# Performance work log

Measured on AMD Instinct MI355X. Metric: run time of the kernel, lower is better.

The kernel has to match this reference:

```python
import jax, jax.numpy as jnp
import numpy as np

B, H, M, TK, NK, D = 4, 8, 1, 512, 511, 512
HD = D // H
NEG_INF = float('-inf')


def setup_inputs() -> dict:
    key = jax.random.key(0)
    ks = jax.random.split(key, 8)
    s = 0.02
    leaves = jax.random.normal(ks[0], (B, M, TK, D), jnp.float32)
    nodes = jax.random.normal(ks[1], (B, M, NK, D), jnp.float32)
    # per-head [left, right] leaf span of each tree node, left <= right
    node_indices = jnp.sort(jax.random.randint(ks[2], (B, H, M, NK, 2), 0, TK), axis=-1)
    key_pad = jnp.zeros((B, M, TK), jnp.bool_)
    node_pad = jnp.zeros((B, M, NK), jnp.bool_)
    Wq = jax.random.normal(ks[3], (D, D), jnp.float32) * s
    Wk = jax.random.normal(ks[4], (D, D), jnp.float32) * s
    Wv = jax.random.normal(ks[5], (D, D), jnp.float32) * s
    Wo = jax.random.normal(ks[6], (D, D), jnp.float32) * s
    bq = jnp.zeros((D,), jnp.float32)
    bk = jnp.zeros((D,), jnp.float32)
    bv = jnp.zeros((D,), jnp.float32)
    bo = jnp.zeros((D,), jnp.float32)
    return dict(leaves=leaves, nodes=nodes, Wq=Wq, Wk=Wk, Wv=Wv, Wo=Wo,
                bq=bq, bk=bk, bv=bv, bo=bo,
                node_indices=node_indices, key_pad=key_pad, node_pad=node_pad)


def _build_masks(node_indices, key_pad, node_pad):
    """Faithful jnp port of WeightMaskEff.build_mask_leaves_subtree."""
    L = M * (TK + NK)
    rg = jnp.arange(TK)
    # --- leaf queries: attend only non-pad leaves (node keys fully masked) ---
    leaf_mask = jnp.concatenate([key_pad, jnp.ones_like(node_pad)], axis=2)
    leaf_mask = leaf_mask.reshape(B, 1, 1, 1, L)                       # (B,1,1,1,L)
    # --- node queries over leaf keys: leaves inside the node's span ---
    idx_q = jnp.swapaxes(node_indices, 2, 3)                           # (B,H,NK,M,2)
    lo = idx_q[..., 0][..., None, None]                                # (B,H,NK,M,1,1)
    hi = idx_q[..., 1][..., None, None]
    leave_npad = (rg < lo) | (rg > hi)                                 # (B,H,NK,M,1,TK)
    leave_npad = leave_npad | jnp.swapaxes(node_pad, 1, 2)[:, None, :, :, None, None]
    leaf_keys_mask = leave_npad | key_pad[:, None, None, None, :, :]   # (B,H,NK,M,M,TK)
    # --- node queries over node keys: span overlap, lower-triangular ---
    in_span = (rg >= node_indices[..., 0:1]) & (rg <= node_indices[..., 1:2])  # (B,H,M,NK,TK)
    nl = in_span.astype(jnp.float32)
    overlap = jnp.tril(jnp.clip(jnp.einsum('bhmit,bhmjt->bhmij', nl, nl), 0.0, 1.0)) > 0
    node_npad = jnp.swapaxes(overlap[:, :, :, :, None, :], 2, 3)       # (B,H,NK,M,1,NK)
    node_keys_mask = (~node_npad) | node_pad[:, None, None, None, :, :]  # (B,H,NK,M,M,NK)
    node_mask = jnp.concatenate([leaf_keys_mask, node_keys_mask], axis=5).reshape(B, H, NK, M, L)
    return leaf_mask, node_mask


def _attention(leaves, nodes, Wq, Wk, Wv, Wo, bq, bk, bv, bo,
               node_indices, key_pad, node_pad):
    TKNK = TK + NK
    L = M * TKNK
    kv_src = jnp.concatenate([leaves, nodes], axis=2)        # (B,M,TKNK,D): key layout [m, tknk]
    q_src = jnp.swapaxes(kv_src, 1, 2).reshape(B, L, D)      # query layout [tknk, m]
    kv = kv_src.reshape(B, L, D)
    q = (q_src @ Wq.T + bq) * (HD ** -0.5)
    k = kv @ Wk.T + bk
    v = kv @ Wv.T + bv
    split = lambda x: jnp.swapaxes(x.reshape(B, L, H, HD), 1, 2)  # (B,H,L,HD)
    qh, kh, vh = split(q), split(k), split(v)
    w = jnp.einsum('bhqd,bhkd->bhqk', qh, kh).reshape(B, H, TKNK, M, L)
    leaf_mask, node_mask = _build_masks(node_indices, key_pad, node_pad)
    w = jnp.concatenate([
        jnp.where(leaf_mask, NEG_INF, w[:, :, :TK]),
        jnp.where(node_mask, NEG_INF, w[:, :, TK:]),
    ], axis=2).reshape(B, H, L, L)
    p = jax.nn.softmax(w, axis=-1)
    out = jnp.einsum('bhqk,bhkd->bhqd', p, vh)
    out = jnp.swapaxes(out, 1, 2).reshape(B, L, D)
    return out @ Wo.T + bo


def reference(leaves, nodes, Wq, Wk, Wv, Wo, bq, bk, bv, bo,
              node_indices, key_pad, node_pad):
    return _attention(leaves, nodes, Wq, Wk, Wv, Wo, bq, bk, bv, bo,
                      node_indices, key_pad, node_pad)
```

## Files before the change

kernel.cpp:

```cpp
#include <hip/hip_runtime.h>
#include <math.h>

#define Bn 4
#define Hn 8
#define TKn 512
#define NKn 511
#define Dn 512
#define HDn 64
#define Ln 1023
#define ROWSn (Bn * Ln)
#define NEG_SENT (-1.0e30f)

typedef __attribute__((ext_vector_type(8))) short short8;
typedef __attribute__((ext_vector_type(4))) short short4v;
typedef __attribute__((ext_vector_type(4))) float f32x4;
typedef unsigned short ushort_t;

__device__ __forceinline__ ushort_t f2bf(float f) {
    union { float f; unsigned int u; } v; v.f = f;
    unsigned int r = v.u + 0x7FFF + ((v.u >> 16) & 1);
    return (ushort_t)(r >> 16);
}
__device__ __forceinline__ unsigned int pk2(float a, float b) {
    return (unsigned int)f2bf(a) | ((unsigned int)f2bf(b) << 16);
}

#define LEAF_U ((Bn * TKn * Dn) / 8)
#define NODE_U ((Bn * NKn * Dn) / 8)
#define W_U    ((Dn * Dn) / 8)
__global__ __launch_bounds__(256) void convert_kernel(
    const float* __restrict__ leaves, const float* __restrict__ nodes,
    const float* __restrict__ Wq, const float* __restrict__ Wk,
    const float* __restrict__ Wv, const float* __restrict__ Wo,
    ushort_t* __restrict__ Xb, ushort_t* __restrict__ Wb)
{
    int u = blockIdx.x * 256 + threadIdx.x;
    const float* src;
    ushort_t* dst;
    if (u < LEAF_U) {
        int e = u * 8;
        int b = e / (TKn * Dn);
        int rem = e - b * (TKn * Dn);
        src = leaves + e;
        dst = Xb + (size_t)b * Ln * Dn + rem;
    } else if (u < LEAF_U + NODE_U) {
        int e = (u - LEAF_U) * 8;
        int b = e / (NKn * Dn);
        int rem = e - b * (NKn * Dn);
        src = nodes + e;
        dst = Xb + ((size_t)b * Ln + TKn) * Dn + rem;
    } else {
        int e = u - LEAF_U - NODE_U;
        int w = e / W_U;
        int rem = (e - w * W_U) * 8;
        src = (w == 0 ? Wq : w == 1 ? Wk : w == 2 ? Wv : Wo) + rem;
        dst = Wb + (size_t)w * Dn * Dn + rem;
    }
    float4 f0 = *(const float4*)src;
    float4 f1 = *(const float4*)(src + 4);
    int4 o;
    o.x = (int)pk2(f0.x, f0.y);
    o.y = (int)pk2(f0.z, f0.w);
    o.z = (int)pk2(f1.x, f1.y);
    o.w = (int)pk2(f1.z, f1.w);
    *(int4*)dst = o;
}

__global__ __launch_bounds__(256) void qkv_mfma_kernel(
    const ushort_t* __restrict__ Xb, const ushort_t* __restrict__ Wb,
    const float* __restrict__ bq, const float* __restrict__ bk, const float* __restrict__ bv,
    ushort_t* __restrict__ Qo, ushort_t* __restrict__ Ko, ushort_t* __restrict__ Vt)
{
    const int col0g = blockIdx.y * 64;
    const int which = col0g >> 9;
    const int colm  = col0g & 511;
    const ushort_t* __restrict__ W = Wb + (size_t)which * Dn * Dn;
    const float* __restrict__ bias = (which == 0) ? bq : (which == 1) ? bk : bv;
    const float scale = (which == 0) ? 0.125f : 1.0f;

    __shared__ ushort_t As[128][72];
    __shared__ ushort_t Bs[64][72];

    const int tid = threadIdx.x;
    const int lane = tid & 63, wave = tid >> 6;
    const int ln = lane & 15, quad = lane >> 4;
    const int wm = wave & 1, wn = wave >> 1;
    const int row0 = blockIdx.x * 128;

    f32x4 acc[2][4];
    #pragma unroll
    for (int i = 0; i < 2; ++i)
        #pragma unroll
        for (int j = 0; j < 4; ++j) acc[i][j] = (f32x4){0.f, 0.f, 0.f, 0.f};

    for (int k0 = 0; k0 < Dn; k0 += 64) {
        #pragma unroll
        for (int s = 0; s < 4; ++s) {
            int e = tid + s * 256;
            int r = e >> 3, c = (e & 7) * 8;
            int row = row0 + r;
            *(int4*)&As[r][c] = (row < ROWSn)
                ? *(const int4*)&Xb[(size_t)row * Dn + k0 + c] : (int4){0, 0, 0, 0};
        }
        #pragma unroll
        for (int s = 0; s < 2; ++s) {
            int e = tid + s * 256;
            int r = e >> 3, c = (e & 7) * 8;
            *(int4*)&Bs[r][c] = *(const int4*)&W[(size_t)(colm + r) * Dn + k0 + c];
        }
        __syncthreads();

        #pragma unroll
        for (int kc = 0; kc < 2; ++kc) {
            short8 af[2], bf[4];
            #pragma unroll
            for (int ni = 0; ni < 2; ++ni)
                af[ni] = *(const short8*)&Bs[wn * 32 + ni * 16 + ln][kc * 32 + quad * 8];
            #pragma unroll
            for (int mi = 0; mi < 4; ++mi)
                bf[mi] = *(const short8*)&As[wm * 64 + mi * 16 + ln][kc * 32 + quad * 8];
            #pragma unroll
            for (int ni = 0; ni < 2; ++ni)
                #pragma unroll
                for (int mi = 0; mi < 4; ++mi)
                    acc[ni][mi] = __builtin_amdgcn_mfma_f32_16x16x32_bf16(af[ni], bf[mi], acc[ni][mi], 0, 0, 0);
        }
        __syncthreads();
    }

    if (which == 2) {
        const int h = colm >> 6;
        #pragma unroll
        for (int ni = 0; ni < 2; ++ni) {
            const int d0 = wn * 32 + ni * 16 + quad * 4;
            const float4 b4 = *(const float4*)&bias[colm + d0];
            #pragma unroll
            for (int mi = 0; mi < 4; ++mi) {
                int row = row0 + wm * 64 + mi * 16 + ln;
                if (row >= ROWSn) continue;
                int bb = row / Ln;
                int l  = row - bb * Ln;
                size_t vbase = ((size_t)((bb * Hn + h) * HDn + d0)) * 1024 + l;
                Vt[vbase]        = f2bf(acc[ni][mi][0] + b4.x);
                Vt[vbase + 1024] = f2bf(acc[ni][mi][1] + b4.y);
                Vt[vbase + 2048] = f2bf(acc[ni][mi][2] + b4.z);
                Vt[vbase + 3072] = f2bf(acc[ni][mi][3] + b4.w);
            }
        }
    } else {
        ushort_t* __restrict__ Y = (which == 0) ? Qo : Ko;
        #pragma unroll
        for (int ni = 0; ni < 2; ++ni) {
            const int colb = colm + wn * 32 + ni * 16 + quad * 4;
            const float4 b4 = *(const float4*)&bias[colb];
            #pragma unroll
            for (int mi = 0; mi < 4; ++mi) {
                int row = row0 + wm * 64 + mi * 16 + ln;
                if (row >= ROWSn) continue;
                uint2 o;
                o.x = pk2(scale * (acc[ni][mi][0] + b4.x), scale * (acc[ni][mi][1] + b4.y));
                o.y = pk2(scale * (acc[ni][mi][2] + b4.z), scale * (acc[ni][mi][3] + b4.w));
                *(uint2*)&Y[(size_t)row * Dn + colb] = o;
            }
        }
    }
}

__global__ __launch_bounds__(256) void outproj_mfma_kernel(
    const ushort_t* __restrict__ AOb, const ushort_t* __restrict__ Wb,
    const float* __restrict__ bo, float* __restrict__ out)
{
    const ushort_t* __restrict__ W = Wb + (size_t)3 * Dn * Dn;
    __shared__ ushort_t As[64][136];
    __shared__ ushort_t Bs[64][136];

    const int tid = threadIdx.x;
    const int lane = tid & 63, wave = tid >> 6;
    const int ln = lane & 15, quad = lane >> 4;
    const int wm = wave & 1, wn = wave >> 1;
    const int row0 = blockIdx.x * 64;
    const int col0 = blockIdx.y * 64;

    f32x4 acc[2][2];
    #pragma unroll
    for (int i = 0; i < 2; ++i)
        #pragma unroll
        for (int j = 0; j < 2; ++j) acc[i][j] = (f32x4){0.f, 0.f, 0.f, 0.f};

    for (int k0 = 0; k0 < Dn; k0 += 128) {
        #pragma unroll
        for (int s = 0; s < 4; ++s) {
            int e = tid + s * 256;
            int r = e >> 4, c = (e & 15) * 8;
            int row = row0 + r;
            *(int4*)&As[r][c] = (row < ROWSn)
                ? *(const int4*)&AOb[(size_t)row * Dn + k0 + c] : (int4){0, 0, 0, 0};
            *(int4*)&Bs[r][c] = *(const int4*)&W[(size_t)(col0 + r) * Dn + k0 + c];
        }
        __syncthreads();

        #pragma unroll
        for (int kc = 0; kc < 4; ++kc) {
            short8 af[2], bf[2];
            #pragma unroll
            for (int ni = 0; ni < 2; ++ni)
                af[ni] = *(const short8*)&Bs[wn * 32 + ni * 16 + ln][kc * 32 + quad * 8];
            #pragma unroll
            for (int mi = 0; mi < 2; ++mi)
                bf[mi] = *(const short8*)&As[wm * 32 + mi * 16 + ln][kc * 32 + quad * 8];
            #pragma unroll
            for (int ni = 0; ni < 2; ++ni)
                #pragma unroll
                for (int mi = 0; mi < 2; ++mi)
                    acc[ni][mi] = __builtin_amdgcn_mfma_f32_16x16x32_bf16(af[ni], bf[mi], acc[ni][mi], 0, 0, 0);
        }
        __syncthreads();
    }

    #pragma unroll
    for (int ni = 0; ni < 2; ++ni) {
        const int colb = col0 + wn * 32 + ni * 16 + quad * 4;
        const float4 b4 = *(const float4*)&bo[colb];
        #pragma unroll
        for (int mi = 0; mi < 2; ++mi) {
            int row = row0 + wm * 32 + mi * 16 + ln;
            if (row >= ROWSn) continue;
            float4 o;
            o.x = acc[ni][mi][0] + b4.x;
            o.y = acc[ni][mi][1] + b4.y;
            o.z = acc[ni][mi][2] + b4.z;
            o.w = acc[ni][mi][3] + b4.w;
            *(float4*)&out[(size_t)row * Dn + colb] = o;
        }
    }
}

__global__ __launch_bounds__(256) void attn_mfma_kernel(
    const ushort_t* __restrict__ Qb, const ushort_t* __restrict__ Kb,
    const ushort_t* __restrict__ Vt, const int* __restrict__ nodeidx,
    ushort_t* __restrict__ AOb)
{
    const int qtile = 15 - (int)blockIdx.x;
    const int h = blockIdx.y, b = blockIdx.z;
    const int tid = threadIdx.x;
    const int lane = tid & 63, wave = tid >> 6;
    const int ln = lane & 15, quad = lane >> 4;
    const bool leafq = qtile < 8;
    const int ktend = leafq ? 8 : qtile + 1;

    __shared__ ushort_t Ks[64][72];
    __shared__ ushort_t Vts[64][72];
    __shared__ int2 nsp[512];

    const int nbase = (b * Hn + h) * NKn * 2;
    if (!leafq) {
        int i = tid;
        nsp[i] = (i < NKn) ? *(const int2*)&nodeidx[nbase + 2 * i] : (int2){0, -1};
        i = tid + 256;
        nsp[i] = (i < NKn) ? *(const int2*)&nodeidx[nbase + 2 * i] : (int2){0, -1};
    }

    const int q0 = qtile * 64;
    const int rq = q0 + wave * 16 + ln;
    const ushort_t* qp = Qb + ((size_t)(b * Ln + rq)) * Dn + h * HDn + quad * 8;
    const short8 qf0 = *(const short8*)qp;
    const short8 qf1 = *(const short8*)(qp + 32);

    const bool qvalid = rq < Ln;
    const int iq = rq - TKn;
    int qlo = 0, qhi = -1;
    if (!leafq && qvalid) {
        int2 t = *(const int2*)&nodeidx[nbase + 2 * iq];
        qlo = t.x; qhi = t.y;
    }

    float m_run = NEG_SENT, l_run = 0.f;
    f32x4 O[4];
    #pragma unroll
    for (int nd = 0; nd < 4; ++nd) O[nd] = (f32x4){0.f, 0.f, 0.f, 0.f};

    const size_t kbgl = (size_t)(b * Ln) * Dn + h * HDn;
    const ushort_t* Vp = Vt + (size_t)((b * Hn + h) * HDn) * 1024;

    for (int kt = 0; kt < ktend; ++kt) {
        const int k0 = kt * 64;
        if (kt) __syncthreads();
        #pragma unroll
        for (int s = 0; s < 2; ++s) {
            int e = tid + s * 256;
            int r = e >> 3, c = (e & 7) * 8;
            int key = k0 + r;
            *(int4*)&Ks[r][c] = (key < Ln)
                ? *(const int4*)&Kb[kbgl + (size_t)key * Dn + c] : (int4){0, 0, 0, 0};
            *(int4*)&Vts[r][c] = *(const int4*)&Vp[(size_t)r * 1024 + k0 + c];
        }
        __syncthreads();

        f32x4 st[4];
        #pragma unroll
        for (int n = 0; n < 4; ++n) {
            short8 kf0 = *(const short8*)&Ks[n * 16 + ln][quad * 8];
            short8 kf1 = *(const short8*)&Ks[n * 16 + ln][32 + quad * 8];
            f32x4 s = __builtin_amdgcn_mfma_f32_16x16x32_bf16(kf0, qf0,
                        (f32x4){0.f, 0.f, 0.f, 0.f}, 0, 0, 0);
            st[n] = __builtin_amdgcn_mfma_f32_16x16x32_bf16(kf1, qf1, s, 0, 0, 0);
        }

        if (!leafq) {
            if (k0 < TKn) {
                #pragma unroll
                for (int n = 0; n < 4; ++n) {
                    int keyb = k0 + n * 16 + quad * 4;
                    #pragma unroll
                    for (int r = 0; r < 4; ++r) {
                        int key = keyb + r;
                        bool a = (key >= qlo) && (key <= qhi);
                        st[n][r] = a ? st[n][r] : NEG_SENT;
                    }
                }
            } else {
                #pragma unroll
                for (int n = 0; n < 4; ++n) {
                    int idx = k0 + n * 16 + quad * 4 - TKn;
                    int4 sa = *(const int4*)&nsp[idx];
                    int4 sb = *(const int4*)&nsp[idx + 2];
                    bool a0 = (idx + 0 <= iq) && (sa.x <= qhi) && (qlo <= sa.y);
                    bool a1 = (idx + 1 <= iq) && (sa.z <= qhi) && (qlo <= sa.w);
                    bool a2 = (idx + 2 <= iq) && (sb.x <= qhi) && (qlo <= sb.y);
                    bool a3 = (idx + 3 <= iq) && (sb.z <= qhi) && (qlo <= sb.w);
                    st[n][0] = a0 ? st[n][0] : NEG_SENT;
                    st[n][1] = a1 ? st[n][1] : NEG_SENT;
                    st[n][2] = a2 ? st[n][2] : NEG_SENT;
                    st[n][3] = a3 ? st[n][3] : NEG_SENT;
                }
            }
        }

        float mx = NEG_SENT;
        #pragma unroll
        for (int n = 0; n < 4; ++n)
            #pragma unroll
            for (int r = 0; r < 4; ++r) mx = fmaxf(mx, st[n][r]);
        mx = fmaxf(mx, __shfl_xor(mx, 16));
        mx = fmaxf(mx, __shfl_xor(mx, 32));

        float mn = fmaxf(m_run, mx);
        float alpha = __expf(m_run - mn);
        m_run = mn;

        float lsum = 0.f;
        short4v ap[4];
        #pragma unroll
        for (int n = 0; n < 4; ++n) {
            float p[4];
            #pragma unroll
            for (int r = 0; r < 4; ++r) {
                float sv = st[n][r];
                p[r] = (sv == NEG_SENT) ? 0.f : __expf(sv - mn);
                lsum += p[r];
            }
            ap[n] = (short4v){(short)f2bf(p[0]), (short)f2bf(p[1]),
                              (short)f2bf(p[2]), (short)f2bf(p[3])};
        }
        lsum += __shfl_xor(lsum, 16);
        lsum += __shfl_xor(lsum, 32);
        l_run = l_run * alpha + lsum;

        float alr[4];
        #pragma unroll
        for (int r = 0; r < 4; ++r) alr[r] = __shfl(alpha, quad * 4 + r);
        #pragma unroll
        for (int nd = 0; nd < 4; ++nd)
            #pragma unroll
            for (int r = 0; r < 4; ++r) O[nd][r] *= alr[r];

        #pragma unroll
        for (int c = 0; c < 4; ++c) {
            #pragma unroll
            for (int nd = 0; nd < 4; ++nd) {
                short4v bv = *(const short4v*)&Vts[nd * 16 + ln][c * 16 + quad * 4];
                O[nd] = __builtin_amdgcn_mfma_f32_16x16x16bf16_1k(ap[c], bv, O[nd], 0, 0, 0);
            }
        }
    }

    float lr[4];
    #pragma unroll
    for (int r = 0; r < 4; ++r) lr[r] = __shfl(l_run, quad * 4 + r);
    #pragma unroll
    for (int r = 0; r < 4; ++r) {
        int rqr = q0 + wave * 16 + quad * 4 + r;
        if (rqr >= Ln) continue;
        float inv = 1.f / lr[r];
        size_t base = (size_t)(b * Ln + rqr) * Dn + h * HDn;
        #pragma unroll
        for (int nd = 0; nd < 4; ++nd)
            AOb[base + nd * 16 + ln] = f2bf(O[nd][r] * inv);
    }
}

extern "C" void kernel_launch(void* const* d_in, const int* in_sizes, int n_in,
                              void* d_out, int out_size, void* d_ws, size_t ws_size,
                              hipStream_t stream)
{
    const float* leaves = (const float*)d_in[0];
    const float* nodes  = (const float*)d_in[1];
    const float* Wq = (const float*)d_in[2];
    const float* Wk = (const float*)d_in[3];
    const float* Wv = (const float*)d_in[4];
    const float* Wo = (const float*)d_in[5];
    const float* bq = (const float*)d_in[6];
    const float* bk = (const float*)d_in[7];
    const float* bv = (const float*)d_in[8];
    const float* bo = (const float*)d_in[9];
    const int* nodeidx = (const int*)d_in[10];

    ushort_t* ws = (ushort_t*)d_ws;
    const size_t N = (size_t)ROWSn * Dn;
    ushort_t* Xb  = ws;
    ushort_t* Wb  = Xb + N;
    ushort_t* Qb  = Wb + (size_t)4 * Dn * Dn;
    ushort_t* Kb  = Qb + N;
    ushort_t* Vt  = Kb + N;
    ushort_t* AOb = Vt + (size_t)Bn * Hn * HDn * 1024;

    convert_kernel<<<1535, 256, 0, stream>>>(leaves, nodes, Wq, Wk, Wv, Wo, Xb, Wb);

    dim3 pgrid(32, 24);
    qkv_mfma_kernel<<<pgrid, 256, 0, stream>>>(Xb, Wb, bq, bk, bv, Qb, Kb, Vt);

    dim3 agrid(16, Hn, Bn);
    attn_mfma_kernel<<<agrid, 256, 0, stream>>>(Qb, Kb, Vt, nodeidx, AOb);

    dim3 ogrid(64, 8);
    outproj_mfma_kernel<<<ogrid, 256, 0, stream>>>(AOb, Wb, bo, (float*)d_out);
}
```

Baseline: 156.2 us.

## Split attention key tiles across waves with 16-row query blocks and XCD-aware mapping

The attention kernel now gives each block 16 query rows instead of 64. Its four waves split the key tiles among themselves, flash-decoding style, and their partial max, sum and O values are merged through shared memory at the end. K and V fragments are read straight from global memory, so the shared-memory staging and the per-tile barriers are gone. The 1D grid of 2048 blocks is mapped so that each XCD handles a few (batch, head) pairs, which should help L2 reuse and balance work across causal tiles. The cost is more total global/L2 traffic, since K and V are reloaded per block with no LDS reuse, plus a shared-memory reduction epilogue.

```diff
diff --git a/kernel.cpp b/kernel.cpp
--- a/kernel.cpp
+++ b/kernel.cpp
@@ -240,17 +240,21 @@
     const ushort_t* __restrict__ Vt, const int* __restrict__ nodeidx,
     ushort_t* __restrict__ AOb)
 {
-    const int qtile = 15 - (int)blockIdx.x;
-    const int h = blockIdx.y, b = blockIdx.z;
+    const int lb = blockIdx.x;
+    const int xcd = lb & 7, u = lb >> 3;
+    const int bh = xcd * 4 + (u >> 6);
+    const int qg = 63 - (u & 63);
+    const int b = bh >> 3, h = bh & 7;
     const int tid = threadIdx.x;
     const int lane = tid & 63, wave = tid >> 6;
     const int ln = lane & 15, quad = lane >> 4;
-    const bool leafq = qtile < 8;
-    const int ktend = leafq ? 8 : qtile + 1;
-
-    __shared__ ushort_t Ks[64][72];
-    __shared__ ushort_t Vts[64][72];
+    const int q0 = qg * 16;
+    const bool leafq = q0 < TKn;
+    const int ktend = leafq ? 8 : ((q0 + 16 + 63) >> 6);
+
     __shared__ int2 nsp[512];
+    __shared__ float Osh[4][64][17];
+    __shared__ float msh[4][16], lsh[4][16];
 
     const int nbase = (b * Hn + h) * NKn * 2;
     if (!leafq) {
@@ -258,11 +262,12 @@
         nsp[i] = (i < NKn) ? *(const int2*)&nodeidx[nbase + 2 * i] : (int2){0, -1};
         i = tid + 256;
         nsp[i] = (i < NKn) ? *(const int2*)&nodeidx[nbase + 2 * i] : (int2){0, -1};
-    }
-
-    const int q0 = qtile * 64;
-    const int rq = q0 + wave * 16 + ln;
-    const ushort_t* qp = Qb + ((size_t)(b * Ln + rq)) * Dn + h * HDn + quad * 8;
+        __syncthreads();
+    }
+
+    const int rq = q0 + ln;
+    const int rqc = (rq < Ln) ? rq : (Ln - 1);
+    const ushort_t* qp = Qb + ((size_t)(b * Ln + rqc)) * Dn + h * HDn + quad * 8;
     const short8 qf0 = *(const short8*)qp;
     const short8 qf1 = *(const short8*)(qp + 32);
 
@@ -279,28 +284,20 @@
     #pragma unroll
     for (int nd = 0; nd < 4; ++nd) O[nd] = (f32x4){0.f, 0.f, 0.f, 0.f};
 
-    const size_t kbgl = (size_t)(b * Ln) * Dn + h * HDn;
+    const ushort_t* Kp = Kb + (size_t)(b * Ln) * Dn + h * HDn;
     const ushort_t* Vp = Vt + (size_t)((b * Hn + h) * HDn) * 1024;
 
-    for (int kt = 0; kt < ktend; ++kt) {
+    for (int kt = wave; kt < ktend; kt += 4) {
         const int k0 = kt * 64;
-        if (kt) __syncthreads();
-        #pragma unroll
-        for (int s = 0; s < 2; ++s) {
-            int e = tid + s * 256;
-            int r = e >> 3, c = (e & 7) * 8;
-            int key = k0 + r;
-            *(int4*)&Ks[r][c] = (key < Ln)
-                ? *(const int4*)&Kb[kbgl + (size_t)key * Dn + c] : (int4){0, 0, 0, 0};
-            *(int4*)&Vts[r][c] = *(const int4*)&Vp[(size_t)r * 1024 + k0 + c];
-        }
-        __syncthreads();
 
         f32x4 st[4];
         #pragma unroll
         for (int n = 0; n < 4; ++n) {
-            short8 kf0 = *(const short8*)&Ks[n * 16 + ln][quad * 8];
-            short8 kf1 = *(const short8*)&Ks[n * 16 + ln][32 + quad * 8];
+            int krow = k0 + n * 16 + ln;
+            if (krow > Ln - 1) krow = Ln - 1;
+            const ushort_t* kp = Kp + (size_t)krow * Dn + quad * 8;
+            short8 kf0 = *(const short8*)kp;
+            short8 kf1 = *(const short8*)(kp + 32);
             f32x4 s = __builtin_amdgcn_mfma_f32_16x16x32_bf16(kf0, qf0,
                         (f32x4){0.f, 0.f, 0.f, 0.f}, 0, 0, 0);
             st[n] = __builtin_amdgcn_mfma_f32_16x16x32_bf16(kf1, qf1, s, 0, 0, 0);
@@ -378,24 +375,34 @@
         for (int c = 0; c < 4; ++c) {
             #pragma unroll
             for (int nd = 0; nd < 4; ++nd) {
-                short4v bv = *(const short4v*)&Vts[nd * 16 + ln][c * 16 + quad * 4];
+                short4v bv = *(const short4v*)&Vp[(size_t)(nd * 16 + ln) * 1024
+                                                  + k0 + c * 16 + quad * 4];
                 O[nd] = __builtin_amdgcn_mfma_f32_16x16x16bf16_1k(ap[c], bv, O[nd], 0, 0, 0);
             }
         }
     }
 
-    float lr[4];
-    #pragma unroll
-    for (int r = 0; r < 4; ++r) lr[r] = __shfl(l_run, quad * 4 + r);
-    #pragma unroll
-    for (int r = 0; r < 4; ++r) {
-        int rqr = q0 + wave * 16 + quad * 4 + r;
-        if (rqr >= Ln) continue;
-        float inv = 1.f / lr[r];
-        size_t base = (size_t)(b * Ln + rqr) * Dn + h * HDn;
-        #pragma unroll
-        for (int nd = 0; nd < 4; ++nd)
-            AOb[base + nd * 16 + ln] = f2bf(O[nd][r] * inv);
+    if (lane < 16) { msh[wave][lane] = m_run; lsh[wave][lane] = l_run; }
+    #pragma unroll
+    for (int nd = 0; nd < 4; ++nd)
+        #pragma unroll
+        for (int r = 0; r < 4; ++r)
+            Osh[wave][nd * 16 + ln][quad * 4 + r] = O[nd][r];
+    __syncthreads();
+
+    const int d = tid & 63;
+    #pragma unroll
+    for (int qq = tid >> 6; qq < 16; qq += 4) {
+        int rqq = q0 + qq;
+        if (rqq >= Ln) continue;
+        float m0 = msh[0][qq], m1 = msh[1][qq], m2 = msh[2][qq], m3 = msh[3][qq];
+        float M = fmaxf(fmaxf(m0, m1), fmaxf(m2, m3));
+        float e0 = __expf(m0 - M), e1 = __expf(m1 - M);
+        float e2 = __expf(m2 - M), e3 = __expf(m3 - M);
+        float L = lsh[0][qq] * e0 + lsh[1][qq] * e1 + lsh[2][qq] * e2 + lsh[3][qq] * e3;
+        float acc = Osh[0][d][qq] * e0 + Osh[1][d][qq] * e1
+                  + Osh[2][d][qq] * e2 + Osh[3][d][qq] * e3;
+        AOb[(size_t)(b * Ln + rqq) * Dn + h * HDn + d] = f2bf(acc / L);
     }
 }
 
@@ -429,8 +436,7 @@
     dim3 pgrid(32, 24);
     qkv_mfma_kernel<<<pgrid, 256, 0, stream>>>(Xb, Wb, bq, bk, bv, Qb, Kb, Vt);
 
-    dim3 agrid(16, Hn, Bn);
-    attn_mfma_kernel<<<agrid, 256, 0, stream>>>(Qb, Kb, Vt, nodeidx, AOb);
+    attn_mfma_kernel<<<2048, 256, 0, stream>>>(Qb, Kb, Vt, nodeidx, AOb);
 
     dim3 ogrid(64, 8);
     outproj_mfma_kernel<<<ogrid, 256, 0, stream>>>(AOb, Wb, bo, (float*)d_out);
```

Result: slower. 185.7 us (+18.9%).

## Double-buffer K/V tiles with register prefetch and split attention into smaller blocks

Applied to the files above, without the earlier changes.

The attention kernel now uses 128-thread blocks over 32-query tiles, launched as a flat grid of 1024 blocks with the heaviest tiles scheduled first. K/V tiles are prefetched into registers one step ahead and stored into double-buffered shared memory, so each iteration needs one barrier instead of two and global loads overlap with MFMA work. The shared-memory row padding changes to 70, and the convert kernel now zeroes the padding column of the transposed V buffer. The aim is more blocks for load balancing across CUs and hidden load latency, at the cost of higher register pressure and K/V reloaded once per 32 queries instead of per 64.

```diff
diff --git a/kernel.cpp b/kernel.cpp
--- a/kernel.cpp
+++ b/kernel.cpp
@@ -32,9 +32,11 @@
     const float* __restrict__ leaves, const float* __restrict__ nodes,
     const float* __restrict__ Wq, const float* __restrict__ Wk,
     const float* __restrict__ Wv, const float* __restrict__ Wo,
-    ushort_t* __restrict__ Xb, ushort_t* __restrict__ Wb)
+    ushort_t* __restrict__ Xb, ushort_t* __restrict__ Wb,
+    ushort_t* __restrict__ Vtz)
 {
     int u = blockIdx.x * 256 + threadIdx.x;
+    if (u < Bn * Hn * HDn) Vtz[(size_t)u * 1024 + 1023] = 0;
     const float* src;
     ushort_t* dst;
     if (u < LEAF_U) {
@@ -235,34 +237,39 @@
     }
 }
 
-__global__ __launch_bounds__(256) void attn_mfma_kernel(
+__global__ __launch_bounds__(128) void attn_mfma_kernel(
     const ushort_t* __restrict__ Qb, const ushort_t* __restrict__ Kb,
     const ushort_t* __restrict__ Vt, const int* __restrict__ nodeidx,
     ushort_t* __restrict__ AOb)
 {
-    const int qtile = 15 - (int)blockIdx.x;
-    const int h = blockIdx.y, b = blockIdx.z;
+    const int bid = blockIdx.x;
+    const int bh = bid & 31;
+    const int qt = 31 - (bid >> 5);
+    const int b = bh >> 3, h = bh & 7;
     const int tid = threadIdx.x;
     const int lane = tid & 63, wave = tid >> 6;
     const int ln = lane & 15, quad = lane >> 4;
-    const bool leafq = qtile < 8;
-    const int ktend = leafq ? 8 : qtile + 1;
-
-    __shared__ ushort_t Ks[64][72];
-    __shared__ ushort_t Vts[64][72];
+    const bool leafq = qt < 16;
+    const int ktend = leafq ? 8 : (qt / 2 + 1);
+
+    __shared__ ushort_t Ks[2][64][70];
+    __shared__ ushort_t Vts[2][64][70];
     __shared__ int2 nsp[512];
 
     const int nbase = (b * Hn + h) * NKn * 2;
     if (!leafq) {
-        int i = tid;
-        nsp[i] = (i < NKn) ? *(const int2*)&nodeidx[nbase + 2 * i] : (int2){0, -1};
-        i = tid + 256;
-        nsp[i] = (i < NKn) ? *(const int2*)&nodeidx[nbase + 2 * i] : (int2){0, -1};
-    }
-
-    const int q0 = qtile * 64;
-    const int rq = q0 + wave * 16 + ln;
-    const ushort_t* qp = Qb + ((size_t)(b * Ln + rq)) * Dn + h * HDn + quad * 8;
+        #pragma unroll
+        for (int s = 0; s < 4; ++s) {
+            int idx = tid + s * 128;
+            nsp[idx] = (idx < NKn) ? *(const int2*)&nodeidx[nbase + 2 * idx]
+                                   : (int2){0, -1};
+        }
+    }
+
+    const int q0 = qt * 32 + wave * 16;
+    const int rq = q0 + ln;
+    const int rqc = (rq < Ln) ? rq : (Ln - 1);
+    const ushort_t* qp = Qb + ((size_t)(b * Ln + rqc)) * Dn + h * HDn + quad * 8;
     const short8 qf0 = *(const short8*)qp;
     const short8 qf1 = *(const short8*)(qp + 32);
 
@@ -274,33 +281,51 @@
         qlo = t.x; qhi = t.y;
     }
 
+    const int r0 = tid >> 3;
+    const int c0 = (tid & 7) * 8;
+    const ushort_t* Kp = Kb + (size_t)(b * Ln) * Dn + h * HDn;
+    const ushort_t* Vp = Vt + (size_t)((b * Hn + h) * HDn) * 1024;
+
+    int4 kreg[4], vreg[4];
+    #pragma unroll
+    for (int s = 0; s < 4; ++s) {
+        int r = r0 + 16 * s;
+        int krow = r; if (krow > Ln - 1) krow = Ln - 1;
+        kreg[s] = *(const int4*)&Kp[(size_t)krow * Dn + c0];
+        vreg[s] = *(const int4*)&Vp[(size_t)r * 1024 + c0];
+    }
+
     float m_run = NEG_SENT, l_run = 0.f;
     f32x4 O[4];
     #pragma unroll
     for (int nd = 0; nd < 4; ++nd) O[nd] = (f32x4){0.f, 0.f, 0.f, 0.f};
 
-    const size_t kbgl = (size_t)(b * Ln) * Dn + h * HDn;
-    const ushort_t* Vp = Vt + (size_t)((b * Hn + h) * HDn) * 1024;
-
+    int cur = 0;
     for (int kt = 0; kt < ktend; ++kt) {
         const int k0 = kt * 64;
-        if (kt) __syncthreads();
-        #pragma unroll
-        for (int s = 0; s < 2; ++s) {
-            int e = tid + s * 256;
-            int r = e >> 3, c = (e & 7) * 8;
-            int key = k0 + r;
-            *(int4*)&Ks[r][c] = (key < Ln)
-                ? *(const int4*)&Kb[kbgl + (size_t)key * Dn + c] : (int4){0, 0, 0, 0};
-            *(int4*)&Vts[r][c] = *(const int4*)&Vp[(size_t)r * 1024 + k0 + c];
+
+        #pragma unroll
+        for (int s = 0; s < 4; ++s) {
+            *(int4*)&Ks[cur][r0 + 16 * s][c0] = kreg[s];
+            *(int4*)&Vts[cur][r0 + 16 * s][c0] = vreg[s];
+        }
+        if (kt + 1 < ktend) {
+            const int k1 = k0 + 64;
+            #pragma unroll
+            for (int s = 0; s < 4; ++s) {
+                int r = r0 + 16 * s;
+                int krow = k1 + r; if (krow > Ln - 1) krow = Ln - 1;
+                kreg[s] = *(const int4*)&Kp[(size_t)krow * Dn + c0];
+                vreg[s] = *(const int4*)&Vp[(size_t)r * 1024 + k1 + c0];
+            }
         }
         __syncthreads();
 
         f32x4 st[4];
         #pragma unroll
         for (int n = 0; n < 4; ++n) {
-            short8 kf0 = *(const short8*)&Ks[n * 16 + ln][quad * 8];
-            short8 kf1 = *(const short8*)&Ks[n * 16 + ln][32 + quad * 8];
+            short8 kf0 = *(const short8*)&Ks[cur][n * 16 + ln][quad * 8];
+            short8 kf1 = *(const short8*)&Ks[cur][n * 16 + ln][32 + quad * 8];
             f32x4 s = __builtin_amdgcn_mfma_f32_16x16x32_bf16(kf0, qf0,
                         (f32x4){0.f, 0.f, 0.f, 0.f}, 0, 0, 0);
             st[n] = __builtin_amdgcn_mfma_f32_16x16x32_bf16(kf1, qf1, s, 0, 0, 0);
@@ -378,10 +403,11 @@
         for (int c = 0; c < 4; ++c) {
             #pragma unroll
             for (int nd = 0; nd < 4; ++nd) {
-                short4v bv = *(const short4v*)&Vts[nd * 16 + ln][c * 16 + quad * 4];
+                short4v bv = *(const short4v*)&Vts[cur][nd * 16 + ln][c * 16 + quad * 4];
                 O[nd] = __builtin_amdgcn_mfma_f32_16x16x16bf16_1k(ap[c], bv, O[nd], 0, 0, 0);
             }
         }
+        cur ^= 1;
     }
 
     float lr[4];
@@ -389,7 +415,7 @@
     for (int r = 0; r < 4; ++r) lr[r] = __shfl(l_run, quad * 4 + r);
     #pragma unroll
     for (int r = 0; r < 4; ++r) {
-        int rqr = q0 + wave * 16 + quad * 4 + r;
+        int rqr = q0 + quad * 4 + r;
         if (rqr >= Ln) continue;
         float inv = 1.f / lr[r];
         size_t base = (size_t)(b * Ln + rqr) * Dn + h * HDn;
@@ -424,13 +450,12 @@
     ushort_t* Vt  = Kb + N;
     ushort_t* AOb = Vt + (size_t)Bn * Hn * HDn * 1024;
 
-    convert_kernel<<<1535, 256, 0, stream>>>(leaves, nodes, Wq, Wk, Wv, Wo, Xb, Wb);
+    convert_kernel<<<1535, 256, 0, stream>>>(leaves, nodes, Wq, Wk, Wv, Wo, Xb, Wb, Vt);
 
     dim3 pgrid(32, 24);
     qkv_mfma_kernel<<<pgrid, 256, 0, stream>>>(Xb, Wb, bq, bk, bv, Qb, Kb, Vt);
 
-    dim3 agrid(16, Hn, Bn);
-    attn_mfma_kernel<<<agrid, 256, 0, stream>>>(Qb, Kb, Vt, nodeidx, AOb);
+    attn_mfma_kernel<<<1024, 128, 0, stream>>>(Qb, Kb, Vt, nodeidx, AOb);
 
     dim3 ogrid(64, 8);
     outproj_mfma_kernel<<<ogrid, 256, 0, stream>>>(AOb, Wb, bo, (float*)d_out);
```

Result: slower. 177.4 us (+13.6%).
